# Optimization experiments

Measured on AMD Instinct MI355X. Metric: run time of the kernel, lower is better.

## Reference

```python
import jax, jax.numpy as jnp
import numpy as np

BN_EPS = 1e-5

def _bn(x, p):
    # p: [4, C] = (gamma, beta, running_mean, running_var); inference-mode BN
    g, b, m, v = p[0], p[1], p[2], p[3]
    if x.ndim == 3:  # [B, C, N]
        g, b, m, v = g[:, None], b[:, None], m[:, None], v[:, None]
    return g * (x - m) * jax.lax.rsqrt(v + BN_EPS) + b

def _angle_density(xyz, npoints=32):
    # xyz: [B, N, 3]; pairwise cosine distance via a single GEMM instead of expand
    inner = jnp.einsum('bnc,bmc->bnm', xyz, xyz)            # [B, N, N]
    nrm = jnp.sqrt(jnp.sum(xyz * xyz, axis=-1))             # [B, N]
    dist = 1.0 - inner / (nrm[:, :, None] * nrm[:, None, :])
    neg_vals, _ = jax.lax.top_k(-dist, npoints)             # k smallest distances
    feat_density = jnp.mean(-neg_vals, axis=-1)             # [B, N]
    inv = 1.0 / feat_density
    return inv / jnp.max(inv)                               # global max, as in torch

def _density_attn(x, density, wqk, wt, bt, bnp):
    # x: [B, C, N]; density: [B, 1, N]; wqk: [C//4, 1] (q_conv and k_conv share weights)
    xk = wqk * density                                      # [B, C//4, N] (1x1 conv, 1 in-ch)
    energy = jnp.einsum('bdn,bdm->bnm', xk, xk)             # x_q == x_k.T (shared weight)
    attn = jax.nn.softmax(energy, axis=-1)
    attn = attn / (1e-9 + jnp.sum(attn, axis=1, keepdims=True))
    x_r = jnp.einsum('bcn,bnm->bcm', x, attn)               # [B, C, N]
    y = jnp.einsum('oc,bcn->bon', wt, x - x_r) + bt[:, None]
    return x + jax.nn.relu(_bn(y, bnp))

def _conv_bn_relu(x, w, bnp):
    return jax.nn.relu(_bn(jnp.einsum('oc,bcn->bon', w, x), bnp))

def _forward(x, w1, w2, w3, w4, w5, bn1, bn2, bn3, bn4, bn5,
             da1_wqk, da1_wt, da1_bt, da1_bn,
             da2_wqk, da2_wt, da2_bt, da2_bn,
             da3_wqk, da3_wt, da3_bt, da3_bn,
             da4_wqk, da4_wt, da4_bt, da4_bn,
             lin1_w, bn6, lin2_w, lin2_b):
    dens = _angle_density(jnp.transpose(x, (0, 2, 1)), 32)[:, None, :]  # [B, 1, N]
    h = _conv_bn_relu(x, w1, bn1)
    h = _density_attn(h, dens, da1_wqk, da1_wt, da1_bt, da1_bn)
    h = _conv_bn_relu(h, w2, bn2)
    h = _density_attn(h, dens, da2_wqk, da2_wt, da2_bt, da2_bn)
    h = _conv_bn_relu(h, w3, bn3)
    h = _density_attn(h, dens, da3_wqk, da3_wt, da3_bt, da3_bn)
    h = _conv_bn_relu(h, w4, bn4)
    h = _density_attn(h, dens, da4_wqk, da4_wt, da4_bt, da4_bn)
    h = _conv_bn_relu(h, w5, bn5)                           # [B, 1024, N]
    h = jnp.max(h, axis=-1)                                 # adaptive_max_pool1d -> [B, 1024]
    h = jax.nn.relu(_bn(h @ lin1_w.T, bn6))                 # [B, 512]; dropout is identity in eval
    return h @ lin2_w.T + lin2_b                            # [B, num_classes]

def setup_inputs() -> dict:
    key = jax.random.key(0)
    ki = iter(jax.random.split(key, 80))
    def rn(shape, s):
        return jax.random.normal(next(ki), shape, jnp.float32) * s
    def bnp(c):
        return jnp.stack([
            jax.random.uniform(next(ki), (c,), jnp.float32, 0.5, 1.5),  # gamma
            rn((c,), 0.05),                                             # beta
            rn((c,), 0.1),                                              # running_mean
            jax.random.uniform(next(ki), (c,), jnp.float32, 0.5, 1.5),  # running_var
        ])
    B, N, E = 16, 2048, 1024
    d = {}
    d['x'] = jax.random.normal(next(ki), (B, 3, N), jnp.float32)
    d['w1'] = rn((64, 3), 0.5)
    d['w2'] = rn((64, 64), 0.125)
    d['w3'] = rn((64, 64), 0.125)
    d['w4'] = rn((128, 64), 0.125)
    d['w5'] = rn((E, 128), 0.09)
    d['bn1'], d['bn2'], d['bn3'] = bnp(64), bnp(64), bnp(64)
    d['bn4'], d['bn5'] = bnp(128), bnp(E)
    for i, c in zip((1, 2, 3, 4), (64, 64, 64, 128)):
        d[f'da{i}_wqk'] = rn((c // 4, 1), 1.0)
        d[f'da{i}_wt'] = rn((c, c), 1.0 / np.sqrt(c))
        d[f'da{i}_bt'] = rn((c,), 0.05)
        d[f'da{i}_bn'] = bnp(c)
    d['lin1_w'] = rn((512, E), 1.0 / np.sqrt(E))
    d['bn6'] = bnp(512)
    d['lin2_w'] = rn((40, 512), 1.0 / np.sqrt(512))
    d['lin2_b'] = rn((40,), 0.05)
    return d

def reference(x, w1, w2, w3, w4, w5, bn1, bn2, bn3, bn4, bn5,
              da1_wqk, da1_wt, da1_bt, da1_bn,
              da2_wqk, da2_wt, da2_bt, da2_bn,
              da3_wqk, da3_wt, da3_bt, da3_bn,
              da4_wqk, da4_wt, da4_bt, da4_bn,
              lin1_w, bn6, lin2_w, lin2_b):
    return _forward(x, w1, w2, w3, w4, w5, bn1, bn2, bn3, bn4, bn5,
                    da1_wqk, da1_wt, da1_bt, da1_bn,
                    da2_wqk, da2_wt, da2_bt, da2_bn,
                    da3_wqk, da3_wt, da3_bt, da3_bn,
                    da4_wqk, da4_wt, da4_bt, da4_bn,
                    lin1_w, bn6, lin2_w, lin2_b)
```

## Files before the change

### kernel.cpp

```cpp
#include <hip/hip_runtime.h>
#include <math.h>

#define BB 16
#define NN 2048
#define BN_EPS_ 1e-5f

typedef __attribute__((ext_vector_type(8))) short short8v;
typedef __attribute__((ext_vector_type(4))) float f32x4;

__device__ __forceinline__ unsigned short f2bf(float x){
  unsigned u = __float_as_uint(x);
  u += 0x7fffu + ((u >> 16) & 1u);
  return (unsigned short)(u >> 16);
}
__device__ __forceinline__ float bf2f(unsigned short h){
  return __uint_as_float(((unsigned)h) << 16);
}

#define DG 8
__global__ __launch_bounds__(512) void density7_kernel(const float* __restrict__ x,
        float* __restrict__ inv, float* __restrict__ blockmax){
  __shared__ float us0[NN], us1[NN], us2[NN];
  __shared__ unsigned int hist[DG][256];
  __shared__ float buf[DG][128];
  __shared__ unsigned int bufcnt[DG];
  __shared__ unsigned int bB[DG], bC0[DG];
  __shared__ float partial[DG][8];
  __shared__ float rowiv[DG];
  const int b = blockIdx.y;
  const float* xb = x + (size_t)b*3*NN;
  const int t = threadIdx.x;
  {
    float4 v0 = ((const float4*)xb)[t];
    float4 v1 = ((const float4*)(xb + NN))[t];
    float4 v2 = ((const float4*)(xb + 2*NN))[t];
    float4 rr;
    rr.x = rsqrtf(v0.x*v0.x + v1.x*v1.x + v2.x*v2.x);
    rr.y = rsqrtf(v0.y*v0.y + v1.y*v1.y + v2.y*v2.y);
    rr.z = rsqrtf(v0.z*v0.z + v1.z*v1.z + v2.z*v2.z);
    rr.w = rsqrtf(v0.w*v0.w + v1.w*v1.w + v2.w*v2.w);
    v0.x*=rr.x; v0.y*=rr.y; v0.z*=rr.z; v0.w*=rr.w;
    v1.x*=rr.x; v1.y*=rr.y; v1.z*=rr.z; v1.w*=rr.w;
    v2.x*=rr.x; v2.y*=rr.y; v2.z*=rr.z; v2.w*=rr.w;
    ((float4*)us0)[t] = v0; ((float4*)us1)[t] = v1; ((float4*)us2)[t] = v2;
  }
  #pragma unroll
  for (int i = 0; i < 4; ++i) ((unsigned*)hist)[t + 512*i] = 0u;
  if (t < DG) bufcnt[t] = 0u;
  __syncthreads();
  float m0[4], m1[4], m2[4];
  #pragma unroll
  for (int i = 0; i < 4; ++i){
    int c = t + 512*i;
    m0[i] = us0[c]; m1[i] = us1[c]; m2[i] = us2[c];
  }
  const int r0 = blockIdx.x * DG;
  float dd[DG][4]; unsigned qp[DG];
  #pragma unroll
  for (int j = 0; j < DG; ++j){
    float ru0 = us0[r0+j], ru1 = us1[r0+j], ru2 = us2[r0+j];
    unsigned q0 = 0u;
    #pragma unroll
    for (int i = 0; i < 4; ++i){
      float d = 1.0f - (ru0*m0[i] + ru1*m1[i] + ru2*m2[i]);
      dd[j][i] = d;
      int q = (int)(d * 128.0f);
      q = q < 0 ? 0 : (q > 255 ? 255 : q);
      q0 |= (unsigned)q << (8*i);
      atomicAdd(&hist[j][q], 1u);
    }
    qp[j] = q0;
  }
  __syncthreads();

  const int wave = t >> 6, lane = t & 63;
  {
    const int j = wave;
    uint4 cc = *(const uint4*)&hist[j][lane*4];
    unsigned tl = cc.x + cc.y + cc.z + cc.w;
    unsigned inc = tl;
    #pragma unroll
    for (int off = 1; off < 64; off <<= 1){
      unsigned o = __shfl_up(inc, off);
      if (lane >= off) inc += o;
    }
    unsigned base = inc - tl;
    if (base < 32u && base + tl >= 32u){
      unsigned cum = base;
      if (cum < 32u && cum + cc.x >= 32u){ bB[j] = lane*4 + 0; bC0[j] = cum; } cum += cc.x;
      if (cum < 32u && cum + cc.y >= 32u){ bB[j] = lane*4 + 1; bC0[j] = cum; } cum += cc.y;
      if (cum < 32u && cum + cc.z >= 32u){ bB[j] = lane*4 + 2; bC0[j] = cum; } cum += cc.z;
      if (cum < 32u && cum + cc.w >= 32u){ bB[j] = lane*4 + 3; bC0[j] = cum; } cum += cc.w;
    }
  }
  __syncthreads();

  #pragma unroll
  for (int j = 0; j < DG; ++j){
    const int B = (int)bB[j];
    float s = 0.0f;
    #pragma unroll
    for (int i = 0; i < 4; ++i){
      float d = dd[j][i];
      int q = (int)((qp[j] >> (8*i)) & 255u);
      if (q < B) s += d;
      else if (q == B){
        unsigned slot = atomicAdd(&bufcnt[j], 1u);
        if (slot < 128u) buf[j][slot] = d;
      }
    }
    #pragma unroll
    for (int off = 32; off > 0; off >>= 1) s += __shfl_xor(s, off);
    if (lane == 0) partial[j][wave] = s;
  }
  __syncthreads();

  {
    const int j = wave;
    float total = 0.0f;
    #pragma unroll
    for (int wv = 0; wv < 8; ++wv) total += partial[j][wv];
    int cnt = (int)bufcnt[j]; if (cnt > 128) cnt = 128;
    const int rr = 32 - (int)bC0[j];
    float v1 = (lane      < cnt) ? buf[j][lane]      : 0.0f;
    float v2 = (lane + 64 < cnt) ? buf[j][lane + 64] : 0.0f;
    int rk1 = 0, rk2 = 0;
    for (int k = 0; k < cnt; ++k){
      float vk = buf[j][k];
      rk1 += ((vk < v1) || (vk == v1 && k < lane)) ? 1 : 0;
      rk2 += ((vk < v2) || (vk == v2 && k < lane + 64)) ? 1 : 0;
    }
    float contrib = ((lane      < cnt) && (rk1 < rr)) ? v1 : 0.0f;
    contrib      += ((lane + 64 < cnt) && (rk2 < rr)) ? v2 : 0.0f;
    #pragma unroll
    for (int off = 32; off > 0; off >>= 1) contrib += __shfl_xor(contrib, off);
    total += contrib;
    if (lane == 0){
      float iv = 32.0f / total;
      inv[b*NN + r0 + j] = iv;
      rowiv[j] = iv;
    }
  }
  __syncthreads();
  if (t == 0){
    float m = rowiv[0];
    #pragma unroll
    for (int j = 1; j < DG; ++j) m = fmaxf(m, rowiv[j]);
    blockmax[blockIdx.y * gridDim.x + blockIdx.x] = m;
  }
}

__global__ __launch_bounds__(256) void finalize_max_kernel(const float* __restrict__ blockmax,
        float* __restrict__ maxout){
  __shared__ float pw[4];
  const int t = threadIdx.x;
  float m = 0.0f;
  #pragma unroll
  for (int i = 0; i < 16; ++i) m = fmaxf(m, blockmax[t + 256*i]);
  #pragma unroll
  for (int off = 32; off > 0; off >>= 1) m = fmaxf(m, __shfl_xor(m, off));
  if ((t & 63) == 0) pw[t >> 6] = m;
  __syncthreads();
  if (t == 0) *maxout = fmaxf(fmaxf(pw[0], pw[1]), fmaxf(pw[2], pw[3]));
}

__global__ __launch_bounds__(256) void zrow4_kernel(const float* __restrict__ dens,
      const float* __restrict__ maxval,
      const float* __restrict__ w0, const float* __restrict__ w1,
      const float* __restrict__ w2, const float* __restrict__ w3,
      float* __restrict__ out){
  __shared__ float ds[NN];
  const int b = blockIdx.y, t = threadIdx.x;
  float mx = *maxval;
  float r2 = 1.0f / (mx*mx);
  float s0=0.f, s1=0.f, s2=0.f, s3=0.f;
  for (int k = 0; k < 16; ++k){ float w = w0[k]; s0 += w*w; }
  for (int k = 0; k < 16; ++k){ float w = w1[k]; s1 += w*w; }
  for (int k = 0; k < 16; ++k){ float w = w2[k]; s2 += w*w; }
  for (int k = 0; k < 32; ++k){ float w = w3[k]; s3 += w*w; }
  s0 *= r2; s1 *= r2; s2 *= r2; s3 *= r2;
  #pragma unroll
  for (int i = 0; i < NN/256; ++i) ds[t + 256*i] = dens[b*NN + t + 256*i];
  __syncthreads();
  const int wave = t >> 6, lane = t & 63;
  const int RPB = NN / gridDim.x;
  const int r0 = blockIdx.x * RPB;
  for (int r = r0 + wave; r < r0 + RPB; r += 4){
    float dr = ds[r];
    float a0 = s0*dr, a1 = s1*dr, a2 = s2*dr, a3 = s3*dr;
    float q0=0.f, q1=0.f, q2=0.f, q3=0.f;
    #pragma unroll
    for (int i = 0; i < NN/64; ++i){
      float dm = ds[lane + 64*i];
      q0 += __expf(a0*dm); q1 += __expf(a1*dm);
      q2 += __expf(a2*dm); q3 += __expf(a3*dm);
    }
    #pragma unroll
    for (int off = 32; off > 0; off >>= 1){
      q0 += __shfl_xor(q0, off); q1 += __shfl_xor(q1, off);
      q2 += __shfl_xor(q2, off); q3 += __shfl_xor(q3, off);
    }
    if (lane == 0){
      out[0*(size_t)BB*NN + b*NN + r] = 1.0f/q0;
      out[1*(size_t)BB*NN + b*NN + r] = 1.0f/q1;
      out[2*(size_t)BB*NN + b*NN + r] = 1.0f/q2;
      out[3*(size_t)BB*NN + b*NN + r] = 1.0f/q3;
    }
  }
}

template<int C>
__global__ __launch_bounds__(256, 2) void attn_mfma_kernel(const unsigned short* __restrict__ Ah,
      const unsigned short* __restrict__ Al, const float* __restrict__ dens,
      const float* __restrict__ zinv, const float* __restrict__ wqk, int K,
      const float* __restrict__ maxval, unsigned short* __restrict__ raw){
  constexpr int RA = C + 16;
  constexpr int RH = C / 32;
  __shared__ __align__(16) unsigned short ah[C][64], al[C][64];
  __shared__ __align__(16) unsigned short eh[64][64];
  const int id = blockIdx.x;
  const int b  = (id & 7) + ((id >> 9) << 3);
  const int inner = (id >> 3) & 63;
  const int m0 = (inner & 31) * 64;
  const int nh = inner >> 5;
  const size_t HS = (size_t)BB*RA*NN;
  const int t = threadIdx.x;
  float s = 0.0f;
  for (int k = 0; k < K; ++k){ float w = wqk[k]; s += w*w; }
  { float mx = *maxval; s = s / (mx*mx); }
  const float* db = dens + b*NN;
  const float* zb = zinv + b*NN;
  const unsigned short* Abh = Ah + (size_t)b*C*NN;
  const unsigned short* Abl = Al + (size_t)b*C*NN;
  const int ej = t >> 2, ekq = (t & 3) * 16;
  const float dmj = s * db[m0 + ej];
  const unsigned swe = (unsigned)((ej & 7) << 4);
  const int l = t & 63, w = t >> 6;
  const int rw = w & 1, cw = w >> 1;
  const int fc = l & 15, g = l >> 4;
  const unsigned swr = (unsigned)((fc & 7) << 4);
  short8v ones8, zero8;
  #pragma unroll
  for (int q = 0; q < 8; ++q){ ones8[q] = (short)0x3F80; zero8[q] = 0; }
  f32x4 acc[RH][2], cs[2];
  #pragma unroll
  for (int i = 0; i < RH; ++i){ acc[i][0] = (f32x4){0.f,0.f,0.f,0.f}; acc[i][1] = (f32x4){0.f,0.f,0.f,0.f}; }
  cs[0] = (f32x4){0.f,0.f,0.f,0.f}; cs[1] = (f32x4){0.f,0.f,0.f,0.f};

  for (int n0 = nh*(NN/2); n0 < (nh+1)*(NN/2); n0 += 64){
    __syncthreads();
    #pragma unroll
    for (int i = 0; i < C*8/256; ++i){
      int idx = t + 256*i;
      int row = idx >> 3, c8 = (idx & 7) * 8;
      unsigned off = (unsigned)(row*128) + (((unsigned)(c8*2)) ^ ((unsigned)((row&7)<<4)));
      *(uint4*)((char*)ah + off) = *(const uint4*)(Abh + (size_t)row*NN + n0 + c8);
      *(uint4*)((char*)al + off) = *(const uint4*)(Abl + (size_t)row*NN + n0 + c8);
    }
    {
      unsigned hp[8];
      #pragma unroll
      for (int u = 0; u < 4; ++u){
        float4 dn = *(const float4*)(db + n0 + ekq + u*4);
        float4 zv = *(const float4*)(zb + n0 + ekq + u*4);
        float e0 = zv.x*__expf(dn.x*dmj), e1 = zv.y*__expf(dn.y*dmj);
        float e2 = zv.z*__expf(dn.z*dmj), e3 = zv.w*__expf(dn.w*dmj);
        hp[u*2+0] = (unsigned)f2bf(e0) | ((unsigned)f2bf(e1)<<16);
        hp[u*2+1] = (unsigned)f2bf(e2) | ((unsigned)f2bf(e3)<<16);
      }
      unsigned row = (unsigned)(ej*128);
      unsigned o1 = row + (((unsigned)(ekq*2))      ^ swe);
      unsigned o2 = row + (((unsigned)(ekq*2 + 16)) ^ swe);
      *(uint4*)((char*)eh + o1) = make_uint4(hp[0],hp[1],hp[2],hp[3]);
      *(uint4*)((char*)eh + o2) = make_uint4(hp[4],hp[5],hp[6],hp[7]);
    }
    __syncthreads();
    #pragma unroll
    for (int kk = 0; kk < 2; ++kk){
      unsigned ko = ((unsigned)((kk*32 + g*8)*2)) ^ swr;
      short8v bh[2], ai[RH], au[RH];
      #pragma unroll
      for (int ct = 0; ct < 2; ++ct){
        unsigned eoff = (unsigned)(((2*cw + ct)*16 + fc)*128) + ko;
        bh[ct] = *(const short8v*)((const char*)eh + eoff);
      }
      #pragma unroll
      for (int i = 0; i < RH; ++i){
        unsigned aoff = (unsigned)((rw*(C/2) + i*16 + fc)*128) + ko;
        ai[i] = *(const short8v*)((const char*)ah + aoff);
        au[i] = *(const short8v*)((const char*)al + aoff);
      }
      __builtin_amdgcn_s_setprio(1);
      #pragma unroll
      for (int i = 0; i < RH; ++i){
        #pragma unroll
        for (int ct = 0; ct < 2; ++ct){
          acc[i][ct] = __builtin_amdgcn_mfma_f32_16x16x32_bf16(ai[i], bh[ct], acc[i][ct], 0, 0, 0);
          acc[i][ct] = __builtin_amdgcn_mfma_f32_16x16x32_bf16(au[i], bh[ct], acc[i][ct], 0, 0, 0);
        }
      }
      if (rw == 1){
        short8v ac = (fc == 0) ? ones8 : zero8;
        #pragma unroll
        for (int ct = 0; ct < 2; ++ct)
          cs[ct] = __builtin_amdgcn_mfma_f32_16x16x32_bf16(ac, bh[ct], cs[ct], 0, 0, 0);
      }
      __builtin_amdgcn_s_setprio(0);
    }
  }
  #pragma unroll
  for (int ct = 0; ct < 2; ++ct){
    unsigned short* rb = raw + (size_t)nh*HS + (size_t)b*RA*NN + m0 + (2*cw + ct)*16 + fc;
    #pragma unroll
    for (int i = 0; i < RH; ++i){
      #pragma unroll
      for (int r = 0; r < 4; ++r){
        int row = rw*(C/2) + i*16 + g*4 + r;
        rb[(size_t)row*NN] = f2bf(acc[i][ct][r]);
      }
    }
    if (rw == 1){
      #pragma unroll
      for (int r = 0; r < 4; ++r){
        int row = C + g*4 + r;
        rb[(size_t)row*NN] = f2bf(cs[ct][r]);
      }
    }
  }
}

template<int C, bool TP>
__global__ __launch_bounds__(256) void attn_post_kernel(const float* __restrict__ x,
      const unsigned short* __restrict__ raw, const float* __restrict__ wt,
      const float* __restrict__ bt, const float* __restrict__ bnp,
      float* __restrict__ out, unsigned short* __restrict__ th,
      unsigned short* __restrict__ tl){
  constexpr int RA = C + 16;
  __shared__ float ds[32][68];
  __shared__ float ws[32][C+4];
  __shared__ float cbs[64];
  const int b = blockIdx.y, m0 = blockIdx.x*64, t = threadIdx.x;
  const size_t HS = (size_t)BB*RA*NN;
  const float* xb = x + (size_t)b*C*NN;
  const unsigned short* rb0 = raw + (size_t)b*RA*NN;
  const unsigned short* rb1 = raw + HS + (size_t)b*RA*NN;
  if (t < 64) cbs[t] = 1.0f / (1e-9f + bf2f(rb0[(size_t)C*NN + m0 + t]) + bf2f(rb1[(size_t)C*NN + m0 + t]));
  const int tr = t >> 4, tc = t & 15;
  constexpr int R = C/16;
  float acc[R][4];
  #pragma unroll
  for (int i = 0; i < R; ++i){ acc[i][0]=acc[i][1]=acc[i][2]=acc[i][3]=0.0f; }
  for (int c0 = 0; c0 < C; c0 += 32){
    __syncthreads();
    #pragma unroll
    for (int i = 0; i < 8; ++i){
      int idx = t + 256*i;
      int m = idx & 63, cl = idx >> 6;
      int cc = c0 + cl;
      float rv = bf2f(rb0[cc*NN + m0 + m]) + bf2f(rb1[cc*NN + m0 + m]);
      ds[cl][m] = xb[cc*NN + m0 + m] - rv * cbs[m];
    }
    #pragma unroll
    for (int i = 0; i < C*32/256; ++i){
      int idx = t + 256*i;
      int cl = idx & 31, o = idx >> 5;
      ws[cl][o] = wt[o*C + c0 + cl];
    }
    __syncthreads();
    #pragma unroll
    for (int k = 0; k < 32; ++k){
      float4 e = *(const float4*)&ds[k][tc*4];
      float a[R];
      #pragma unroll
      for (int q = 0; q < R/4; ++q)
        *(float4*)&a[q*4] = *(const float4*)&ws[k][tr*R + q*4];
      #pragma unroll
      for (int i = 0; i < R; ++i){
        acc[i][0] += a[i]*e.x; acc[i][1] += a[i]*e.y;
        acc[i][2] += a[i]*e.z; acc[i][3] += a[i]*e.w;
      }
    }
  }
  #pragma unroll
  for (int i = 0; i < R; ++i){
    int o = tr*R + i;
    float g = bnp[o], be = bnp[C+o], mn = bnp[2*C+o], vv = bnp[3*C+o];
    float sc = g * rsqrtf(vv + BN_EPS_);
    float sh = be - mn*sc;
    float bv = bt[o];
    #pragma unroll
    for (int j = 0; j < 4; ++j){
      float y = acc[i][j] + bv;
      y = sc*y + sh;
      y = fmaxf(y, 0.0f);
      acc[i][j] = xb[o*NN + m0 + tc*4 + j] + y;
    }
    if (!TP)
      *(float4*)&out[((size_t)b*C + o)*NN + m0 + tc*4] =
          make_float4(acc[i][0], acc[i][1], acc[i][2], acc[i][3]);
  }
  if (TP){
    unsigned short* Ts = (unsigned short*)&ws[0][0];
    #pragma unroll
    for (int pass = 0; pass < 2; ++pass){
      __syncthreads();
      #pragma unroll
      for (int q = 0; q < R/2; ++q){
        #pragma unroll
        for (int j = 0; j < 4; ++j){
          int n = tc*4 + j;
          float y0 = acc[2*q][j], y1 = acc[2*q+1][j];
          unsigned short a0 = f2bf(y0), a1 = f2bf(y1);
          unsigned short v0 = pass ? f2bf(y0 - bf2f(a0)) : a0;
          unsigned short v1 = pass ? f2bf(y1 - bf2f(a1)) : a1;
          unsigned off = (unsigned)(n*256) +
              (((unsigned)((tr*R + 2*q)*2)) ^ ((unsigned)((n&7)<<4)));
          *(unsigned*)((char*)Ts + off) = (unsigned)v0 | ((unsigned)v1<<16);
        }
      }
      __syncthreads();
      unsigned short* gout = (pass ? tl : th) + ((size_t)b*NN + m0)*128;
      int n = t >> 2;
      #pragma unroll
      for (int s2 = 0; s2 < 4; ++s2){
        int sl = (t&3)*4 + s2;
        unsigned off = (unsigned)(n*256) + ((unsigned)((sl ^ (n&7)) << 4));
        uint4 v = *(const uint4*)((const char*)Ts + off);
        *(uint4*)(gout + (size_t)n*128 + sl*8) = v;
      }
    }
  }
}

template<int CIN, int COUT>
__global__ __launch_bounds__(256) void conv_bn_relu_kernel(const float* __restrict__ x,
      const float* __restrict__ w, const float* __restrict__ bnp, float* __restrict__ out,
      unsigned short* __restrict__ oh, unsigned short* __restrict__ ol){
  constexpr int CH = (CIN < 32) ? CIN : 32;
  __shared__ float xs[CH][68];
  __shared__ float ws[CH][COUT+4];
  const int b = blockIdx.y, m0 = blockIdx.x*64, t = threadIdx.x;
  const float* xb = x + (size_t)b*CIN*NN;
  const int tr = t >> 4, tc = t & 15;
  constexpr int R = COUT/16;
  float acc[R][4];
  #pragma unroll
  for (int i = 0; i < R; ++i){ acc[i][0]=acc[i][1]=acc[i][2]=acc[i][3]=0.0f; }
  for (int c0 = 0; c0 < CIN; c0 += CH){
    __syncthreads();
    for (int idx = t; idx < CH*64; idx += 256){
      int m = idx & 63, cl = idx >> 6;
      xs[cl][m] = xb[(c0+cl)*NN + m0 + m];
    }
    for (int idx = t; idx < CH*COUT; idx += 256){
      int cl = idx % CH, o = idx / CH;
      ws[cl][o] = w[o*CIN + c0 + cl];
    }
    __syncthreads();
    #pragma unroll
    for (int k = 0; k < CH; ++k){
      float4 e = *(const float4*)&xs[k][tc*4];
      float a[R];
      #pragma unroll
      for (int q = 0; q < R/4; ++q)
        *(float4*)&a[q*4] = *(const float4*)&ws[k][tr*R + q*4];
      #pragma unroll
      for (int i = 0; i < R; ++i){
        acc[i][0] += a[i]*e.x; acc[i][1] += a[i]*e.y;
        acc[i][2] += a[i]*e.z; acc[i][3] += a[i]*e.w;
      }
    }
  }
  #pragma unroll
  for (int i = 0; i < R; ++i){
    int o = tr*R + i;
    float g = bnp[o], be = bnp[COUT+o], mn = bnp[2*COUT+o], vv = bnp[3*COUT+o];
    float sc = g * rsqrtf(vv + BN_EPS_);
    float sh = be - mn*sc;
    float4 r;
    float* rp = &r.x;
    #pragma unroll
    for (int j = 0; j < 4; ++j){
      float y = sc*acc[i][j] + sh;
      rp[j] = fmaxf(y, 0.0f);
    }
    size_t base = ((size_t)b*COUT + o)*NN + m0 + tc*4;
    *(float4*)&out[base] = r;
    unsigned short h0=f2bf(r.x), h1=f2bf(r.y), h2=f2bf(r.z), h3=f2bf(r.w);
    uint2 hp, lp;
    hp.x = (unsigned)h0 | ((unsigned)h1<<16);
    hp.y = (unsigned)h2 | ((unsigned)h3<<16);
    lp.x = (unsigned)f2bf(r.x-bf2f(h0)) | ((unsigned)f2bf(r.y-bf2f(h1))<<16);
    lp.y = (unsigned)f2bf(r.z-bf2f(h2)) | ((unsigned)f2bf(r.w-bf2f(h3))<<16);
    *(uint2*)&oh[base] = hp;
    *(uint2*)&ol[base] = lp;
  }
}

__global__ __launch_bounds__(256, 2) void conv5_mfma_kernel(
      const unsigned short* __restrict__ hTh, const unsigned short* __restrict__ hTl,
      const float* __restrict__ w5, const float* __restrict__ bnp,
      float* __restrict__ pooled){
  __shared__ __align__(16) unsigned short wh[64][128], wl[64][128];
  __shared__ __align__(16) unsigned short hh[64][128], hl[64][128];
  const int id = blockIdx.x;
  const int b  = (id & 7) + ((id >> 9) << 3);
  const int inner = (id >> 3) & 63;
  const int o0 = (inner & 15) * 64;
  const int nb = (inner >> 4) * (NN/4);
  const int t = threadIdx.x;
  const int l = t & 63, w = t >> 6;
  const int rw = w & 1, cw = w >> 1;
  const int fc = l & 15, g = l >> 4;
  const unsigned swr = (unsigned)((fc & 7) << 4);
  #pragma unroll
  for (int i = 0; i < 8; ++i){
    int idx = t + 256*i;
    int row = idx >> 5, c0 = (idx & 31) * 4;
    float4 v = *(const float4*)(w5 + (size_t)(o0 + row)*128 + c0);
    unsigned short h0=f2bf(v.x), h1=f2bf(v.y), h2=f2bf(v.z), h3=f2bf(v.w);
    uint2 hp, lp;
    hp.x = (unsigned)h0 | ((unsigned)h1<<16);
    hp.y = (unsigned)h2 | ((unsigned)h3<<16);
    lp.x = (unsigned)f2bf(v.x-bf2f(h0)) | ((unsigned)f2bf(v.y-bf2f(h1))<<16);
    lp.y = (unsigned)f2bf(v.z-bf2f(h2)) | ((unsigned)f2bf(v.w-bf2f(h3))<<16);
    unsigned off = (unsigned)(row*256) + (((unsigned)(c0*2)) ^ ((unsigned)((row&7)<<4)));
    *(uint2*)((char*)wh + off) = hp;
    *(uint2*)((char*)wl + off) = lp;
  }
  float sc[2][4], sh[2][4];
  #pragma unroll
  for (int i = 0; i < 2; ++i){
    #pragma unroll
    for (int r = 0; r < 4; ++r){
      int o = o0 + rw*32 + i*16 + g*4 + r;
      float gg = bnp[o], be = bnp[1024+o], mn = bnp[2048+o], vv = bnp[3072+o];
      sc[i][r] = gg * rsqrtf(vv + BN_EPS_);
      sh[i][r] = be - mn*sc[i][r];
    }
  }
  float vmax[2][4] = {{0.f,0.f,0.f,0.f},{0.f,0.f,0.f,0.f}};
  const unsigned short* hb = hTh + (size_t)b*NN*128;
  const unsigned short* lb = hTl + (size_t)b*NN*128;
  for (int nt = 0; nt < (NN/4)/64; ++nt){
    const int n0 = nb + nt*64;
    __syncthreads();
    #pragma unroll
    for (int i = 0; i < 4; ++i){
      int idx = t + 256*i;
      int row = idx >> 4, sl = idx & 15;
      unsigned off = (unsigned)(row*256) + ((unsigned)((sl << 4) ^ ((row&7)<<4)));
      *(uint4*)((char*)hh + off) = *(const uint4*)(hb + (size_t)(n0+row)*128 + sl*8);
      *(uint4*)((char*)hl + off) = *(const uint4*)(lb + (size_t)(n0+row)*128 + sl*8);
    }
    __syncthreads();
    f32x4 acc[2][2];
    #pragma unroll
    for (int i = 0; i < 2; ++i){ acc[i][0] = (f32x4){0.f,0.f,0.f,0.f}; acc[i][1] = (f32x4){0.f,0.f,0.f,0.f}; }
    #pragma unroll
    for (int kk = 0; kk < 4; ++kk){
      unsigned ko = ((unsigned)((kk*32 + g*8)*2)) ^ swr;
      short8v aih[2], ail[2], bih[2], bil[2];
      #pragma unroll
      for (int i = 0; i < 2; ++i){
        unsigned aoff = (unsigned)((rw*32 + i*16 + fc)*256) + ko;
        aih[i] = *(const short8v*)((const char*)wh + aoff);
        ail[i] = *(const short8v*)((const char*)wl + aoff);
      }
      #pragma unroll
      for (int ct = 0; ct < 2; ++ct){
        unsigned boff = (unsigned)((cw*32 + ct*16 + fc)*256) + ko;
        bih[ct] = *(const short8v*)((const char*)hh + boff);
        bil[ct] = *(const short8v*)((const char*)hl + boff);
      }
      #pragma unroll
      for (int i = 0; i < 2; ++i){
        #pragma unroll
        for (int ct = 0; ct < 2; ++ct){
          acc[i][ct] = __builtin_amdgcn_mfma_f32_16x16x32_bf16(aih[i], bih[ct], acc[i][ct], 0, 0, 0);
          acc[i][ct] = __builtin_amdgcn_mfma_f32_16x16x32_bf16(aih[i], bil[ct], acc[i][ct], 0, 0, 0);
          acc[i][ct] = __builtin_amdgcn_mfma_f32_16x16x32_bf16(ail[i], bih[ct], acc[i][ct], 0, 0, 0);
        }
      }
    }
    #pragma unroll
    for (int i = 0; i < 2; ++i){
      #pragma unroll
      for (int ct = 0; ct < 2; ++ct){
        #pragma unroll
        for (int r = 0; r < 4; ++r){
          float y = sc[i][r]*acc[i][ct][r] + sh[i][r];
          y = fmaxf(y, 0.0f);
          vmax[i][r] = fmaxf(vmax[i][r], y);
        }
      }
    }
  }
  #pragma unroll
  for (int i = 0; i < 2; ++i){
    #pragma unroll
    for (int r = 0; r < 4; ++r){
      float v = vmax[i][r];
      v = fmaxf(v, __shfl_xor(v, 1));
      v = fmaxf(v, __shfl_xor(v, 2));
      v = fmaxf(v, __shfl_xor(v, 4));
      v = fmaxf(v, __shfl_xor(v, 8));
      if (fc == 0)
        atomicMax((unsigned int*)&pooled[b*1024 + o0 + rw*32 + i*16 + g*4 + r],
                  __float_as_uint(v));
    }
  }
}

__global__ void lin1_kernel(const float* __restrict__ pooled, const float* __restrict__ w,
      const float* __restrict__ bnp, float* __restrict__ out1){
  int tid = blockIdx.x*256 + threadIdx.x;
  int b = tid >> 9, j = tid & 511;
  const float4* p4 = (const float4*)(pooled + b*1024);
  const float4* w4 = (const float4*)(w + j*1024);
  float sum = 0.0f;
  for (int e = 0; e < 256; ++e){
    float4 a = p4[e], c = w4[e];
    sum += a.x*c.x + a.y*c.y + a.z*c.z + a.w*c.w;
  }
  float g = bnp[j], be = bnp[512+j], mn = bnp[2*512+j], vv = bnp[3*512+j];
  float s = g * rsqrtf(vv + BN_EPS_);
  float y = s*sum + (be - mn*s);
  out1[b*512 + j] = fmaxf(y, 0.0f);
}

__global__ void lin2_kernel(const float* __restrict__ h, const float* __restrict__ w,
      const float* __restrict__ bias, float* __restrict__ out){
  int tid = blockIdx.x*64 + threadIdx.x;
  if (tid >= 640) return;
  int b = tid / 40, k = tid % 40;
  const float4* h4 = (const float4*)(h + b*512);
  const float4* w4 = (const float4*)(w + k*512);
  float sum = 0.0f;
  for (int e = 0; e < 128; ++e){
    float4 a = h4[e], c = w4[e];
    sum += a.x*c.x + a.y*c.y + a.z*c.z + a.w*c.w;
  }
  out[tid] = sum + bias[k];
}

extern "C" void kernel_launch(void* const* d_in, const int* in_sizes, int n_in,
                              void* d_out, int out_size, void* d_ws, size_t ws_size,
                              hipStream_t stream){
  (void)in_sizes; (void)n_in; (void)out_size; (void)ws_size;
  const float* x     = (const float*)d_in[0];
  const float* w1    = (const float*)d_in[1];
  const float* w2    = (const float*)d_in[2];
  const float* w3    = (const float*)d_in[3];
  const float* w4    = (const float*)d_in[4];
  const float* w5    = (const float*)d_in[5];
  const float* bn1   = (const float*)d_in[6];
  const float* bn2   = (const float*)d_in[7];
  const float* bn3   = (const float*)d_in[8];
  const float* bn4   = (const float*)d_in[9];
  const float* bn5   = (const float*)d_in[10];
  const float* da_wqk[4] = {(const float*)d_in[11], (const float*)d_in[15], (const float*)d_in[19], (const float*)d_in[23]};
  const float* da_wt[4]  = {(const float*)d_in[12], (const float*)d_in[16], (const float*)d_in[20], (const float*)d_in[24]};
  const float* da_bt[4]  = {(const float*)d_in[13], (const float*)d_in[17], (const float*)d_in[21], (const float*)d_in[25]};
  const float* da_bn[4]  = {(const float*)d_in[14], (const float*)d_in[18], (const float*)d_in[22], (const float*)d_in[26]};
  const float* lin1_w = (const float*)d_in[27];
  const float* bn6    = (const float*)d_in[28];
  const float* lin2_w = (const float*)d_in[29];
  const float* lin2_b = (const float*)d_in[30];

  float* ws = (float*)d_ws;
  float* maxval = ws;
  float* dens   = ws + 64;
  float* zinv4  = dens + BB*NN;
  float* hA     = zinv4 + 4*(size_t)BB*NN;
  float* hB     = hA  + (size_t)BB*64*NN;
  float* h4A    = hB  + (size_t)BB*64*NN;
  unsigned short* raw = (unsigned short*)(h4A + (size_t)BB*128*NN);
  float* pooled = (float*)raw + (size_t)BB*144*NN;
  float* l1o    = pooled + BB*1024;
  float* blockmax = l1o + BB*512;
  unsigned short* Ah = (unsigned short*)(blockmax + 4096);
  unsigned short* Al = Ah + (size_t)BB*128*NN;
  float* h4B    = hA;

  density7_kernel<<<dim3(NN/DG, BB), 512, 0, stream>>>(x, dens, blockmax);
  finalize_max_kernel<<<dim3(1), 256, 0, stream>>>(blockmax, maxval);
  zrow4_kernel<<<dim3(32,BB), 256, 0, stream>>>(dens, maxval,
      da_wqk[0], da_wqk[1], da_wqk[2], da_wqk[3], zinv4);

  conv_bn_relu_kernel<3,64><<<dim3(32,BB),256,0,stream>>>(x, w1, bn1, hA, Ah, Al);

  attn_mfma_kernel<64><<<dim3(1024),256,0,stream>>>(Ah, Al, dens, zinv4, da_wqk[0], 16, maxval, raw);
  attn_post_kernel<64,false><<<dim3(32,BB),256,0,stream>>>(hA, raw, da_wt[0], da_bt[0], da_bn[0], hB, nullptr, nullptr);

  conv_bn_relu_kernel<64,64><<<dim3(32,BB),256,0,stream>>>(hB, w2, bn2, hA, Ah, Al);

  attn_mfma_kernel<64><<<dim3(1024),256,0,stream>>>(Ah, Al, dens, zinv4 + (size_t)BB*NN, da_wqk[1], 16, maxval, raw);
  attn_post_kernel<64,false><<<dim3(32,BB),256,0,stream>>>(hA, raw, da_wt[1], da_bt[1], da_bn[1], hB, nullptr, nullptr);

  conv_bn_relu_kernel<64,64><<<dim3(32,BB),256,0,stream>>>(hB, w3, bn3, hA, Ah, Al);

  attn_mfma_kernel<64><<<dim3(1024),256,0,stream>>>(Ah, Al, dens, zinv4 + 2*(size_t)BB*NN, da_wqk[2], 16, maxval, raw);
  attn_post_kernel<64,false><<<dim3(32,BB),256,0,stream>>>(hA, raw, da_wt[2], da_bt[2], da_bn[2], hB, nullptr, nullptr);

  conv_bn_relu_kernel<64,128><<<dim3(32,BB),256,0,stream>>>(hB, w4, bn4, h4A, Ah, Al);

  attn_mfma_kernel<128><<<dim3(1024),256,0,stream>>>(Ah, Al, dens, zinv4 + 3*(size_t)BB*NN, da_wqk[3], 32, maxval, raw);
  attn_post_kernel<128,true><<<dim3(32,BB),256,0,stream>>>(h4A, raw, da_wt[3], da_bt[3], da_bn[3], h4B, Ah, Al);

  hipMemsetAsync(pooled, 0, BB*1024*sizeof(float), stream);
  conv5_mfma_kernel<<<dim3(1024),256,0,stream>>>(Ah, Al, w5, bn5, pooled);
  lin1_kernel<<<dim3(32),256,0,stream>>>(pooled, lin1_w, bn6, l1o);
  lin2_kernel<<<dim3(10),64,0,stream>>>(l1o, lin2_w, lin2_b, (float*)d_out);
}
```

Before: 498.3 us.

## Compute exp attention operand in registers instead of staging through LDS

The attention MFMA kernel no longer builds the 64x64 bf16 exp tile in shared memory. Each lane now computes its own B-operand fragment with __expf directly before the MFMAs. The column-sum MFMA against a ones vector is replaced by a scalar per-lane sum reduced with cross-lane shuffles, and only the single sum row is written out. This removes LDS writes and reads and an extra MFMA per step. In exchange, both row-half waves now compute the same exponentials, doubling the exp work.

```diff
diff --git a/kernel.cpp b/kernel.cpp
--- a/kernel.cpp
+++ b/kernel.cpp
@@ -217,7 +217,6 @@
   constexpr int RA = C + 16;
   constexpr int RH = C / 32;
   __shared__ __align__(16) unsigned short ah[C][64], al[C][64];
-  __shared__ __align__(16) unsigned short eh[64][64];
   const int id = blockIdx.x;
   const int b  = (id & 7) + ((id >> 9) << 3);
   const int inner = (id >> 3) & 63;
@@ -232,20 +231,17 @@
   const float* zb = zinv + b*NN;
   const unsigned short* Abh = Ah + (size_t)b*C*NN;
   const unsigned short* Abl = Al + (size_t)b*C*NN;
-  const int ej = t >> 2, ekq = (t & 3) * 16;
-  const float dmj = s * db[m0 + ej];
-  const unsigned swe = (unsigned)((ej & 7) << 4);
   const int l = t & 63, w = t >> 6;
   const int rw = w & 1, cw = w >> 1;
   const int fc = l & 15, g = l >> 4;
   const unsigned swr = (unsigned)((fc & 7) << 4);
-  short8v ones8, zero8;
-  #pragma unroll
-  for (int q = 0; q < 8; ++q){ ones8[q] = (short)0x3F80; zero8[q] = 0; }
-  f32x4 acc[RH][2], cs[2];
+  float dm[2];
+  dm[0] = s * db[m0 + (2*cw+0)*16 + fc];
+  dm[1] = s * db[m0 + (2*cw+1)*16 + fc];
+  f32x4 acc[RH][2];
+  float cs[2] = {0.f, 0.f};
   #pragma unroll
   for (int i = 0; i < RH; ++i){ acc[i][0] = (f32x4){0.f,0.f,0.f,0.f}; acc[i][1] = (f32x4){0.f,0.f,0.f,0.f}; }
-  cs[0] = (f32x4){0.f,0.f,0.f,0.f}; cs[1] = (f32x4){0.f,0.f,0.f,0.f};
 
   for (int n0 = nh*(NN/2); n0 < (nh+1)*(NN/2); n0 += 64){
     __syncthreads();
@@ -257,55 +253,55 @@
       *(uint4*)((char*)ah + off) = *(const uint4*)(Abh + (size_t)row*NN + n0 + c8);
       *(uint4*)((char*)al + off) = *(const uint4*)(Abl + (size_t)row*NN + n0 + c8);
     }
-    {
-      unsigned hp[8];
-      #pragma unroll
-      for (int u = 0; u < 4; ++u){
-        float4 dn = *(const float4*)(db + n0 + ekq + u*4);
-        float4 zv = *(const float4*)(zb + n0 + ekq + u*4);
-        float e0 = zv.x*__expf(dn.x*dmj), e1 = zv.y*__expf(dn.y*dmj);
-        float e2 = zv.z*__expf(dn.z*dmj), e3 = zv.w*__expf(dn.w*dmj);
-        hp[u*2+0] = (unsigned)f2bf(e0) | ((unsigned)f2bf(e1)<<16);
-        hp[u*2+1] = (unsigned)f2bf(e2) | ((unsigned)f2bf(e3)<<16);
-      }
-      unsigned row = (unsigned)(ej*128);
-      unsigned o1 = row + (((unsigned)(ekq*2))      ^ swe);
-      unsigned o2 = row + (((unsigned)(ekq*2 + 16)) ^ swe);
-      *(uint4*)((char*)eh + o1) = make_uint4(hp[0],hp[1],hp[2],hp[3]);
-      *(uint4*)((char*)eh + o2) = make_uint4(hp[4],hp[5],hp[6],hp[7]);
-    }
     __syncthreads();
     #pragma unroll
     for (int kk = 0; kk < 2; ++kk){
+      const int kb = n0 + kk*32 + g*8;
+      float4 dn0 = *(const float4*)(db + kb);
+      float4 dn1 = *(const float4*)(db + kb + 4);
+      float4 zv0 = *(const float4*)(zb + kb);
+      float4 zv1 = *(const float4*)(zb + kb + 4);
       unsigned ko = ((unsigned)((kk*32 + g*8)*2)) ^ swr;
-      short8v bh[2], ai[RH], au[RH];
-      #pragma unroll
-      for (int ct = 0; ct < 2; ++ct){
-        unsigned eoff = (unsigned)(((2*cw + ct)*16 + fc)*128) + ko;
-        bh[ct] = *(const short8v*)((const char*)eh + eoff);
-      }
+      short8v ai[RH], au[RH];
       #pragma unroll
       for (int i = 0; i < RH; ++i){
         unsigned aoff = (unsigned)((rw*(C/2) + i*16 + fc)*128) + ko;
         ai[i] = *(const short8v*)((const char*)ah + aoff);
         au[i] = *(const short8v*)((const char*)al + aoff);
       }
-      __builtin_amdgcn_s_setprio(1);
-      #pragma unroll
-      for (int i = 0; i < RH; ++i){
+      #pragma unroll
+      for (int ct = 0; ct < 2; ++ct){
+        float e[8];
+        e[0] = zv0.x*__expf(dn0.x*dm[ct]); e[1] = zv0.y*__expf(dn0.y*dm[ct]);
+        e[2] = zv0.z*__expf(dn0.z*dm[ct]); e[3] = zv0.w*__expf(dn0.w*dm[ct]);
+        e[4] = zv1.x*__expf(dn1.x*dm[ct]); e[5] = zv1.y*__expf(dn1.y*dm[ct]);
+        e[6] = zv1.z*__expf(dn1.z*dm[ct]); e[7] = zv1.w*__expf(dn1.w*dm[ct]);
+        short8v bh;
+        float se = 0.0f;
         #pragma unroll
-        for (int ct = 0; ct < 2; ++ct){
-          acc[i][ct] = __builtin_amdgcn_mfma_f32_16x16x32_bf16(ai[i], bh[ct], acc[i][ct], 0, 0, 0);
-          acc[i][ct] = __builtin_amdgcn_mfma_f32_16x16x32_bf16(au[i], bh[ct], acc[i][ct], 0, 0, 0);
+        for (int j = 0; j < 8; ++j){
+          unsigned short hj = f2bf(e[j]);
+          bh[j] = (short)hj;
+          se += bf2f(hj);
         }
-      }
-      if (rw == 1){
-        short8v ac = (fc == 0) ? ones8 : zero8;
+        if (rw == 1) cs[ct] += se;
+        __builtin_amdgcn_s_setprio(1);
         #pragma unroll
-        for (int ct = 0; ct < 2; ++ct)
-          cs[ct] = __builtin_amdgcn_mfma_f32_16x16x32_bf16(ac, bh[ct], cs[ct], 0, 0, 0);
-      }
-      __builtin_amdgcn_s_setprio(0);
+        for (int i = 0; i < RH; ++i){
+          acc[i][ct] = __builtin_amdgcn_mfma_f32_16x16x32_bf16(ai[i], bh, acc[i][ct], 0, 0, 0);
+          acc[i][ct] = __builtin_amdgcn_mfma_f32_16x16x32_bf16(au[i], bh, acc[i][ct], 0, 0, 0);
+        }
+        __builtin_amdgcn_s_setprio(0);
+      }
+    }
+  }
+  if (rw == 1){
+    #pragma unroll
+    for (int ct = 0; ct < 2; ++ct){
+      float c = cs[ct];
+      c += __shfl_xor(c, 16);
+      c += __shfl_xor(c, 32);
+      cs[ct] = c;
     }
   }
   #pragma unroll
@@ -319,13 +315,8 @@
         rb[(size_t)row*NN] = f2bf(acc[i][ct][r]);
       }
     }
-    if (rw == 1){
-      #pragma unroll
-      for (int r = 0; r < 4; ++r){
-        int row = C + g*4 + r;
-        rb[(size_t)row*NN] = f2bf(cs[ct][r]);
-      }
-    }
+    if (rw == 1 && g == 0)
+      rb[(size_t)C*NN] = f2bf(cs[ct]);
   }
 }
 
```

After: 540.3 us. 8.4% more time.
